# Optimization experiments

Measured on AMD Instinct MI355X. Metric: run time of the kernel, lower is better.

The kernel has to match this reference:

```python
import jax, jax.numpy as jnp
import numpy as np
from jax import lax
import math

C = 32            # num_channles
L_IN = 1024       # input signal length (forced by feature_size=520 constraint)
B = 1024          # batch


def _unfold(x, k, s):
    # x: (B, C, L) -> (B, C, n, k), torch Tensor.unfold(dim=2, size=k, step=s)
    n = (x.shape[-1] - k) // s + 1
    idx = np.arange(n)[:, None] * s + np.arange(k)[None, :]
    return x[..., idx]


def _always(x, w, b):
    # Conv1DAlwaysLayer: beta - sum_k (1 - window)*w, then relu, then leaky_relu(0.02)
    win = _unfold(x, 8, 2)                                  # (B,C,n,8)
    r = b[None, :, None] - jnp.einsum('bcnk,ck->bcn', 1.0 - win, w)
    return jax.nn.leaky_relu(jax.nn.relu(r), 0.02)


def _eventually(x, w, b):
    # Conv1DEventuallyLayer: relu(1 - (beta - sum_k window*w)), then leaky_relu(0.02)
    win = _unfold(x, 8, 2)
    r = 1.0 - (b[None, :, None] - jnp.einsum('bcnk,ck->bcn', win, w))
    return jax.nn.leaky_relu(jax.nn.relu(r), 0.02)


def _bn(x, g, b):
    # BatchNorm1d in training mode: batch statistics over (B, L), biased var
    m = x.mean(axis=(0, 2), keepdims=True)
    v = ((x - m) ** 2).mean(axis=(0, 2), keepdims=True)
    return (x - m) * jax.lax.rsqrt(v + 1e-5) * g[None, :, None] + b[None, :, None]


def _avgpool(x, k, s):
    return _unfold(x, k, s).mean(axis=-1)


def _maxpool(x, k, s):
    return _unfold(x, k, s).max(axis=-1)


def _laplace_filters(la_a, la_b):
    # LaplacePredicate filter bank: (C, 1, 16)
    A, ep, tal, f = 0.08, 0.03, 0.1, 50.0
    w = 2.0 * math.pi * f
    q = 1.0 - ep ** 2
    t = jnp.linspace(0.0, 1.0, 16, dtype=jnp.float32)       # kernel_size -> 16
    p = t[None, :] - (la_b / la_a)                           # (C,16)
    y = A * jnp.exp(-ep / math.sqrt(q) * (w * (p - tal))) * (-jnp.sin(w * (p - tal)))
    return y.reshape(C, 1, 16)


def setup_inputs() -> dict:
    key = jax.random.key(0)
    ks = jax.random.split(key, 32)
    rn = lambda k, shp: jax.random.normal(k, shp, dtype=jnp.float32)
    inp = {
        'x': rn(ks[0], (B, 1, L_IN)),
        # LaplacePredicate params
        'la_a': jnp.linspace(1.0, 10.0, C, dtype=jnp.float32).reshape(C, 1),
        'la_b': jnp.linspace(0.0, 10.0, C, dtype=jnp.float32).reshape(C, 1),
        'la_bias': rn(ks[1], (C,)),
        # BatchNorm after predicate
        'bn1_g': rn(ks[2], (C,)) * 0.1 + 1.0,
        'bn1_b': rn(ks[3], (C,)) * 0.1,
        # conv1d branch: Always -> Eventually -> MaxPool -> BN -> Eventually
        'a1_w': rn(ks[4], (C, 8)), 'a1_b': rn(ks[5], (C,)),
        'e1_w': rn(ks[6], (C, 8)), 'e1_b': rn(ks[7], (C,)),
        'bn2_g': rn(ks[8], (C,)) * 0.1 + 1.0, 'bn2_b': rn(ks[9], (C,)) * 0.1,
        'e2_w': rn(ks[10], (C, 8)), 'e2_b': rn(ks[11], (C,)),
        # conv1dFG branch: Eventually -> Always -> MaxPool -> BN -> Eventually
        'f1_w': rn(ks[12], (C, 8)), 'f1_b': rn(ks[13], (C,)),
        'fa_w': rn(ks[14], (C, 8)), 'fa_b': rn(ks[15], (C,)),
        'bn3_g': rn(ks[16], (C,)) * 0.1 + 1.0, 'bn3_b': rn(ks[17], (C,)) * 0.1,
        'f2_w': rn(ks[18], (C, 8)), 'f2_b': rn(ks[19], (C,)),
        # fc: 768 -> 1024 -> 512 -> 128 -> 10 (W stored (in,out))
        'w1': rn(ks[20], (768, 1024)) * (768 ** -0.5), 'b1': rn(ks[21], (1024,)) * 0.01,
        'w2': rn(ks[22], (1024, 512)) * (1024 ** -0.5), 'b2': rn(ks[23], (512,)) * 0.01,
        'w3': rn(ks[24], (512, 128)) * (512 ** -0.5), 'b3': rn(ks[25], (128,)) * 0.01,
        'w4': rn(ks[26], (128, 10)) * (128 ** -0.5), 'b4': rn(ks[27], (10,)) * 0.01,
    }
    return inp


def _forward(x, la_a, la_b, la_bias, bn1_g, bn1_b,
             a1_w, a1_b, e1_w, e1_b, bn2_g, bn2_b, e2_w, e2_b,
             f1_w, f1_b, fa_w, fa_b, bn3_g, bn3_b, f2_w, f2_b,
             w1, b1, w2, b2, w3, b3, w4, b4):
    # predicate_pos: LaplacePredicate -> BN -> AvgPool(3,2)
    filt = _laplace_filters(la_a, la_b)                      # (32,1,16)
    h = lax.conv_general_dilated(x, filt, window_strides=(1,),
                                 padding=[(16, 16)])         # (B,32,1041)
    h = h + la_bias[None, :, None]
    h = _bn(h, bn1_g, bn1_b)
    h = _avgpool(h, 3, 2)                                    # (B,32,520)
    # NOTE: fuseautoencoder/norm path in the source is dead code (result unused)
    # conv1d branch
    x1 = _always(h, a1_w, a1_b)                              # (B,32,257)
    x1 = _eventually(x1, e1_w, e1_b)                         # (B,32,125)
    x1 = _maxpool(x1, 4, 4)                                  # (B,32,31)
    x1 = _bn(x1, bn2_g, bn2_b)
    x1 = _eventually(x1, e2_w, e2_b)                         # (B,32,12)
    # conv1dFG branch
    x2 = _eventually(h, f1_w, f1_b)
    x2 = _always(x2, fa_w, fa_b)
    x2 = _maxpool(x2, 4, 4)
    x2 = _bn(x2, bn3_g, bn3_b)
    x2 = _eventually(x2, f2_w, f2_b)                         # (B,32,12)
    z = jnp.concatenate([x1, x2], axis=1).reshape(x.shape[0], -1)  # (B,768)
    z = jax.nn.relu(z @ w1 + b1)
    z = jax.nn.relu(z @ w2 + b2)    # Dropout -> identity (eval)
    z = jax.nn.relu(z @ w3 + b3)
    z = jax.nn.relu(z @ w4 + b4)
    return z                                                 # (B,10)


def reference(x, la_a, la_b, la_bias, bn1_g, bn1_b,
              a1_w, a1_b, e1_w, e1_b, bn2_g, bn2_b, e2_w, e2_b,
              f1_w, f1_b, fa_w, fa_b, bn3_g, bn3_b, f2_w, f2_b,
              w1, b1, w2, b2, w3, b3, w4, b4):
    return _forward(x, la_a, la_b, la_bias, bn1_g, bn1_b,
                    a1_w, a1_b, e1_w, e1_b, bn2_g, bn2_b, e2_w, e2_b,
                    f1_w, f1_b, fa_w, fa_b, bn3_g, bn3_b, f2_w, f2_b,
                    w1, b1, w2, b2, w3, b3, w4, b4)
```

## Files before the change

### kernel.cpp

```cpp
#include <hip/hip_runtime.h>
#include <math.h>


#define L_MP 31

using s8v = __attribute__((ext_vector_type(8))) short;
using f4v = __attribute__((ext_vector_type(4))) float;

__device__ __forceinline__ ushort f2bf(float f) {
    unsigned u = __float_as_uint(f);
    u += 0x7fffu + ((u >> 16) & 1u);
    return (ushort)(u >> 16);
}
__device__ __forceinline__ float bf2f(ushort u) {
    return __uint_as_float(((unsigned)u) << 16);
}

__global__ __launch_bounds__(256) void leaf_kernel(
    const float* __restrict__ x, double* __restrict__ xp,
    const float* __restrict__ w1, const float* __restrict__ w2,
    const float* __restrict__ w3,
    ushort* __restrict__ wt1, ushort* __restrict__ wt2, ushort* __restrict__ wt3)
{
    __shared__ __align__(16) float xr[1040];
    __shared__ float wred[4][17];
    __shared__ float tile[32][33];
    int bx = blockIdx.x, tid = threadIdx.x;

    if (bx < 1024) {
        int b = bx;
        for (int i = tid; i < 1024; i += 256) xr[i] = x[b * 1024 + i];
        if (tid < 16) xr[1024 + tid] = 0.f;
        __syncthreads();
        float acc[17];
#pragma unroll
        for (int d = 0; d < 17; ++d) acc[d] = 0.f;
        for (int p = tid; p < 1024; p += 256) {
            float v = xr[p];
            acc[16] += v;
#pragma unroll
            for (int d = 0; d < 16; ++d)
                acc[d] += v * xr[p + d];
        }
#pragma unroll
        for (int off = 32; off >= 1; off >>= 1)
#pragma unroll
            for (int d = 0; d < 17; ++d)
                acc[d] += __shfl_down(acc[d], off);
        int wave = tid >> 6, lane = tid & 63;
        if (lane == 0)
            for (int d = 0; d < 17; ++d) wred[wave][d] = acc[d];
        __syncthreads();
        if (tid < 17) {
            double tot = (double)wred[0][tid] + (double)wred[1][tid]
                       + (double)wred[2][tid] + (double)wred[3][tid];
            xp[tid * 1024 + b] = tot;
        }
    } else {
        int t2 = bx - 1024;
        const float* W; ushort* Wt; int K, N, ntx, tl;
        if (t2 < 768)       { W = w1; Wt = wt1; K = 768;  N = 1024; ntx = 32; tl = t2; }
        else if (t2 < 1280) { W = w2; Wt = wt2; K = 1024; N = 512;  ntx = 16; tl = t2 - 768; }
        else                { W = w3; Wt = wt3; K = 512;  N = 128;  ntx = 4;  tl = t2 - 1280; }
        int n0 = (tl % ntx) * 32, k0 = (tl / ntx) * 32;
        int tx = tid & 31, ty = tid >> 5;
#pragma unroll
        for (int i = 0; i < 4; ++i)
            tile[ty + 8 * i][tx] = W[(size_t)(k0 + ty + 8 * i) * N + n0 + tx];
        __syncthreads();
#pragma unroll
        for (int i = 0; i < 4; ++i)
            Wt[(size_t)(n0 + ty + 8 * i) * K + k0 + tx] = f2bf(tile[tx][ty + 8 * i]);
    }
}

__global__ __launch_bounds__(512) void prep_kernel(
    const double* __restrict__ xp,
    const float* __restrict__ la_a, const float* __restrict__ la_b,
    const float* __restrict__ bn1_g, const float* __restrict__ bn1_b,
    float* __restrict__ g18_out, float* __restrict__ a1d1_out)
{
    __shared__ double stats[17];
    __shared__ float fs[32][16];
    int tid = threadIdx.x, wv = tid >> 6, lane = tid & 63;

    for (int row = wv; row < 17; row += 8) {
        const double* r = xp + (size_t)row * 1024;
        double a = 0.0;
        for (int i = lane; i < 1024; i += 64) a += r[i];
#pragma unroll
        for (int off = 32; off >= 1; off >>= 1) a += __shfl_down(a, off);
        if (lane == 0) stats[row] = a;
    }

    {
        int c = tid >> 4, k = tid & 15;
        const double A = 0.08, ep = 0.03, tal = 0.1;
        const double w = 2.0 * 3.14159265358979323846 * 50.0;
        const double q = 1.0 - ep * ep;
        double t = (double)k / 15.0;
        double p = t - (double)la_b[c] / (double)la_a[c];
        double arg = w * (p - tal);
        double y = A * exp(-ep / sqrt(q) * arg) * (-sin(arg));
        fs[c][k] = (float)y;
    }
    __syncthreads();
    if (tid < 32) {
        int c = tid;
        for (int i = 0; i < 18; ++i) {
            float g = 0.f;
            for (int k = i - 2; k <= i; ++k)
                if (k >= 0 && k < 16) g += fs[c][k];
            g18_out[c * 18 + i] = g;
        }
        double Sf = 0.0;
        for (int k = 0; k < 16; ++k) Sf += (double)fs[c][k];
        double E2 = 0.0;
        for (int k = 0; k < 16; ++k)
            for (int k2 = 0; k2 < 16; ++k2)
                E2 += (double)fs[c][k] * (double)fs[c][k2]
                    * stats[k > k2 ? k - k2 : k2 - k];
        const double N = 1024.0 * 1041.0;
        double Sx = stats[16];
        double mc  = Sx * Sf / N;
        double var = E2 / N - mc * mc;
        double invstd = 1.0 / sqrt(var + 1e-5);
        float alpha = bn1_g[c] * (float)invstd;
        a1d1_out[c]      = alpha / 3.0f;
        a1d1_out[32 + c] = bn1_b[c] - (float)mc * alpha;
    }
}

__global__ __launch_bounds__(256) void branches_kernel(
    const float* __restrict__ x,
    const float* __restrict__ g18g, const float* __restrict__ a1d1,
    const float* __restrict__ a1w_g, const float* __restrict__ a1b_g,
    const float* __restrict__ e1w_g, const float* __restrict__ e1b_g,
    const float* __restrict__ f1w_g, const float* __restrict__ f1b_g,
    const float* __restrict__ faw_g, const float* __restrict__ fab_g,
    float* __restrict__ p1, float* __restrict__ p2)
{
    __shared__ float xs[1140];
    __shared__ float htail[16][6];

    int blk = blockIdx.x;
    int b = blk >> 1, hf = blk & 1;
    int t = threadIdx.x;
    int wv = t >> 6, lane = t & 63;

    {
        float4 v = ((const float4*)(x + (size_t)b * 1024))[t];
        int li = 16 + 4 * t;
        int ph = li + (li >> 4);
        xs[ph] = v.x; xs[ph + 1] = v.y; xs[ph + 2] = v.z; xs[ph + 3] = v.w;
        if (t < 16) xs[t] = 0.f;
        if (t < 32) { int i = 1040 + t; xs[i + (i >> 4)] = 0.f; }
    }
    __syncthreads();

    if (t < 96) {
        int cl = t / 6, e = t - 6 * (t / 6);
        int cg = hf * 16 + cl;
        float s = 0.f;
#pragma unroll
        for (int i = 0; i < 18; ++i) {
            int li = 1024 + 2 * e + i;
            s += g18g[cg * 18 + i] * xs[li + (li >> 4)];
        }
        htail[cl][e] = s * a1d1[cg] + a1d1[32 + cg];
    }
    __syncthreads();

    float xw[32];
    {
        int base = 17 * lane;
#pragma unroll
        for (int q = 0; q < 16; ++q) xw[q] = xs[base + q];
#pragma unroll
        for (int q = 0; q < 16; ++q) xw[16 + q] = xs[base + 17 + q];
    }

    for (int cc = 0; cc < 4; ++cc) {
        int cl = wv * 4 + cc;
        int cg = __builtin_amdgcn_readfirstlane(hf * 16 + cl);
        float alpha = a1d1[cg], delta = a1d1[32 + cg];

        float hv[8];
        {
            float g[18];
#pragma unroll
            for (int i = 0; i < 18; ++i) g[i] = g18g[cg * 18 + i];
#pragma unroll
            for (int jj = 0; jj < 8; ++jj) {
                float s = 0.f;
#pragma unroll
                for (int i = 0; i < 18; ++i) s += g[i] * xw[2 * jj + i];
                hv[jj] = s * alpha + delta;
            }
        }

        float x1v[4], x2v[4];
        {
            float hx[14];
#pragma unroll
            for (int q = 0; q < 8; ++q) hx[q] = hv[q];
#pragma unroll
            for (int q = 0; q < 6; ++q) {
                float u = __shfl_down(hv[q], 1);
                float tl = htail[cl][q];
                hx[8 + q] = (lane == 63) ? tl : u;
            }
            float wa[8], wf[8];
            float A1 = a1b_g[cg], F1 = 1.f - f1b_g[cg];
#pragma unroll
            for (int k = 0; k < 8; ++k) {
                wa[k] = a1w_g[cg * 8 + k];
                wf[k] = f1w_g[cg * 8 + k];
                A1 -= wa[k];
            }
#pragma unroll
            for (int nn = 0; nn < 4; ++nn) {
                float s1 = A1, s2 = F1;
#pragma unroll
                for (int k = 0; k < 8; ++k) {
                    float h = hx[2 * nn + k];
                    s1 += h * wa[k];
                    s2 += h * wf[k];
                }
                x1v[nn] = s1 > 0.f ? s1 : 0.f;
                x2v[nn] = s2 > 0.f ? s2 : 0.f;
            }
        }

        float y1v[2], y2v[2];
        {
            float xx1[10], xx2[10];
#pragma unroll
            for (int q = 0; q < 4; ++q) { xx1[q] = x1v[q]; xx2[q] = x2v[q]; }
#pragma unroll
            for (int q = 0; q < 4; ++q) {
                xx1[4 + q] = __shfl_down(x1v[q], 1);
                xx2[4 + q] = __shfl_down(x2v[q], 1);
            }
#pragma unroll
            for (int q = 0; q < 2; ++q) {
                xx1[8 + q] = __shfl_down(x1v[q], 2);
                xx2[8 + q] = __shfl_down(x2v[q], 2);
            }
            float we[8], wfa[8];
            float E1 = 1.f - e1b_g[cg], FA = fab_g[cg];
#pragma unroll
            for (int k = 0; k < 8; ++k) {
                we[k]  = e1w_g[cg * 8 + k];
                wfa[k] = faw_g[cg * 8 + k];
                FA -= wfa[k];
            }
#pragma unroll
            for (int mm = 0; mm < 2; ++mm) {
                float s1 = E1, s2 = FA;
#pragma unroll
                for (int k = 0; k < 8; ++k) {
                    s1 += xx1[2 * mm + k] * we[k];
                    s2 += xx2[2 * mm + k] * wfa[k];
                }
                y1v[mm] = s1 > 0.f ? s1 : 0.f;
                y2v[mm] = s2 > 0.f ? s2 : 0.f;
            }
        }

        {
            float m1 = fmaxf(y1v[0], y1v[1]);
            float m2 = fmaxf(y2v[0], y2v[1]);
            float n1 = __shfl_down(m1, 1);
            float n2 = __shfl_down(m2, 1);
            int tt = lane >> 1;
            if (!(lane & 1) && tt < L_MP) {
                int bc = b * 32 + hf * 16 + cl;
                p1[(size_t)bc * L_MP + tt] = fmaxf(m1, n1);
                p2[(size_t)bc * L_MP + tt] = fmaxf(m2, n2);
            }
        }
    }
}

__global__ __launch_bounds__(256) void pstats_kernel(
    const float* __restrict__ p1, const float* __restrict__ p2,
    double* __restrict__ bn_d)
{
    __shared__ double wr[4][2];
    int bx = blockIdx.x, arr = bx >> 5, c = bx & 31;
    const float* p = arr ? p2 : p1;
    int t = threadIdx.x, wv = t >> 6, lane = t & 63;
    double s = 0.0, q = 0.0;
    for (int bb = t; bb < 1024; bb += 256) {
        const float* r = p + ((size_t)bb * 32 + c) * L_MP;
#pragma unroll
        for (int j = 0; j < L_MP; ++j) {
            double v = (double)r[j];
            s += v; q += v * v;
        }
    }
#pragma unroll
    for (int off = 32; off >= 1; off >>= 1) {
        s += __shfl_down(s, off);
        q += __shfl_down(q, off);
    }
    if (lane == 0) { wr[wv][0] = s; wr[wv][1] = q; }
    __syncthreads();
    if (t == 0) {
        bn_d[arr * 64 + c]      = wr[0][0] + wr[1][0] + wr[2][0] + wr[3][0];
        bn_d[arr * 64 + 32 + c] = wr[0][1] + wr[1][1] + wr[2][1] + wr[3][1];
    }
}

__global__ __launch_bounds__(256) void final_ev_kernel(
    const float* __restrict__ p1, const float* __restrict__ p2,
    const float* __restrict__ e2w_g, const float* __restrict__ e2b_g,
    const float* __restrict__ f2w_g, const float* __restrict__ f2b_g,
    const double* __restrict__ bn_d,
    const float* __restrict__ bn2_g, const float* __restrict__ bn2_b,
    const float* __restrict__ bn3_g, const float* __restrict__ bn3_b,
    ushort* __restrict__ z0)
{
    __shared__ float pr[2][32][31];
    __shared__ float w2s[2][32][8];
    __shared__ float al[2][32], de[2][32], eb[2][32];
    int b = blockIdx.x, tid = threadIdx.x;
    for (int i = tid; i < 992; i += 256) {
        pr[0][0][i] = p1[b * 992 + i];
        pr[1][0][i] = p2[b * 992 + i];
    }
    {
        w2s[0][0][tid] = e2w_g[tid];
        w2s[1][0][tid] = f2w_g[tid];
    }
    if (tid < 64) {
        int br = tid >> 5, c = tid & 31;
        double sum = bn_d[br * 64 + c], sq = bn_d[br * 64 + 32 + c];
        const double N = 1024.0 * 31.0;
        double mean = sum / N;
        double var = sq / N - mean * mean;
        float g  = br ? bn3_g[c] : bn2_g[c];
        float be = br ? bn3_b[c] : bn2_b[c];
        float alpha = g * (float)(1.0 / sqrt(var + 1e-5));
        al[br][c] = alpha;
        de[br][c] = be - (float)mean * alpha;
        eb[br][c] = br ? f2b_g[c] : e2b_g[c];
    }
    __syncthreads();
    for (int u = tid; u < 768; u += 256) {
        int br = u / 384, rem = u - br * 384;
        int c = rem / 12, tt = rem - c * 12;
        float a = al[br][c], d = de[br][c];
        float s = 1.f - eb[br][c];
#pragma unroll
        for (int k = 0; k < 8; ++k)
            s += (pr[br][c][2 * tt + k] * a + d) * w2s[br][c][k];
        z0[(size_t)b * 768 + u] = f2bf(s > 0.f ? s : 0.f);
    }
}

template<int NT>
__global__ __launch_bounds__(256) void gemm_mfma_kernel(
    const ushort* __restrict__ A, const ushort* __restrict__ Bt,
    const float* __restrict__ bias, ushort* __restrict__ C,
    int N, int K)
{
    int w = blockIdx.x * 4 + (threadIdx.x >> 6);
    int lane = threadIdx.x & 63;
    int nstr = N / (16 * NT);
    int mt = w / nstr, ns = w - mt * nstr;
    int r = lane & 15, q = lane >> 4;
    const ushort* ap = A + (size_t)(mt * 16 + r) * K + q * 8;
    const ushort* bp[NT];
    f4v acc[NT];
#pragma unroll
    for (int u = 0; u < NT; ++u) {
        bp[u] = Bt + (size_t)(ns * 16 * NT + u * 16 + r) * K + q * 8;
        acc[u] = (f4v){0.f, 0.f, 0.f, 0.f};
    }
    int nk = K >> 5;
    s8v a0 = *(const s8v*)ap;
    s8v b0[NT];
#pragma unroll
    for (int u = 0; u < NT; ++u) b0[u] = *(const s8v*)bp[u];
#pragma unroll 4
    for (int i = 0; i < nk; ++i) {
        int j = (i + 1 < nk) ? i + 1 : i;
        s8v a1 = *(const s8v*)(ap + (size_t)j * 32);
        s8v b1[NT];
#pragma unroll
        for (int u = 0; u < NT; ++u) b1[u] = *(const s8v*)(bp[u] + (size_t)j * 32);
#pragma unroll
        for (int u = 0; u < NT; ++u)
            acc[u] = __builtin_amdgcn_mfma_f32_16x16x32_bf16(a0, b0[u], acc[u], 0, 0, 0);
        a0 = a1;
#pragma unroll
        for (int u = 0; u < NT; ++u) b0[u] = b1[u];
    }
    int row0 = mt * 16 + q * 4;
#pragma unroll
    for (int u = 0; u < NT; ++u) {
        int col = ns * 16 * NT + u * 16 + r;
        float bv = bias[col];
#pragma unroll
        for (int rr = 0; rr < 4; ++rr) {
            float v = acc[u][rr] + bv;
            v = v > 0.f ? v : 0.f;
            C[(size_t)(row0 + rr) * N + col] = f2bf(v);
        }
    }
}

__global__ __launch_bounds__(256) void gemm3_fc4_kernel(
    const ushort* __restrict__ A, const ushort* __restrict__ Bt,
    const float* __restrict__ bias, const float* __restrict__ w4,
    const float* __restrict__ b4, float* __restrict__ out)
{
    __shared__ ushort strip[16][132];
    const int K = 512, NCOL = 128;
    int blk = blockIdx.x;
    int wv = threadIdx.x >> 6, lane = threadIdx.x & 63;
    int r = lane & 15, q = lane >> 4;

    const ushort* ap  = A + (size_t)(blk * 16 + r) * K + q * 8;
    const ushort* bp0 = Bt + (size_t)(wv * 32 + r) * K + q * 8;
    const ushort* bp1 = Bt + (size_t)(wv * 32 + 16 + r) * K + q * 8;
    f4v acc0 = {0.f, 0.f, 0.f, 0.f}, acc1 = {0.f, 0.f, 0.f, 0.f};
    int nk = K >> 5;
    s8v a0 = *(const s8v*)ap;
    s8v c0 = *(const s8v*)bp0;
    s8v d0 = *(const s8v*)bp1;
#pragma unroll 4
    for (int i = 0; i < nk; ++i) {
        int j = (i + 1 < nk) ? i + 1 : i;
        s8v a1 = *(const s8v*)(ap + (size_t)j * 32);
        s8v c1 = *(const s8v*)(bp0 + (size_t)j * 32);
        s8v d1 = *(const s8v*)(bp1 + (size_t)j * 32);
        acc0 = __builtin_amdgcn_mfma_f32_16x16x32_bf16(a0, c0, acc0, 0, 0, 0);
        acc1 = __builtin_amdgcn_mfma_f32_16x16x32_bf16(a0, d0, acc1, 0, 0, 0);
        a0 = a1; c0 = c1; d0 = d1;
    }
    float bv0 = bias[wv * 32 + r], bv1 = bias[wv * 32 + 16 + r];
#pragma unroll
    for (int rr = 0; rr < 4; ++rr) {
        float v0 = acc0[rr] + bv0; v0 = v0 > 0.f ? v0 : 0.f;
        float v1 = acc1[rr] + bv1; v1 = v1 > 0.f ? v1 : 0.f;
        strip[q * 4 + rr][wv * 32 + r]      = f2bf(v0);
        strip[q * 4 + rr][wv * 32 + 16 + r] = f2bf(v1);
    }
    __syncthreads();

    int t = threadIdx.x;
    if (t < 160) {
        int m = t / 10, n = t - 10 * (t / 10);
        float a = b4[n];
#pragma unroll 8
        for (int k = 0; k < NCOL; ++k)
            a += bf2f(strip[m][k]) * w4[k * 10 + n];
        out[(size_t)(blk * 16 + m) * 10 + n] = a > 0.f ? a : 0.f;
    }
}

extern "C" void kernel_launch(void* const* d_in, const int* in_sizes, int n_in,
                              void* d_out, int out_size, void* d_ws, size_t ws_size,
                              hipStream_t stream)
{
    (void)in_sizes; (void)n_in; (void)out_size; (void)ws_size;
    const float* x      = (const float*)d_in[0];
    const float* la_a   = (const float*)d_in[1];
    const float* la_b   = (const float*)d_in[2];
    const float* bn1_g  = (const float*)d_in[4];
    const float* bn1_b  = (const float*)d_in[5];
    const float* a1_w   = (const float*)d_in[6];
    const float* a1_b   = (const float*)d_in[7];
    const float* e1_w   = (const float*)d_in[8];
    const float* e1_b   = (const float*)d_in[9];
    const float* bn2_g  = (const float*)d_in[10];
    const float* bn2_b  = (const float*)d_in[11];
    const float* e2_w   = (const float*)d_in[12];
    const float* e2_b   = (const float*)d_in[13];
    const float* f1_w   = (const float*)d_in[14];
    const float* f1_b   = (const float*)d_in[15];
    const float* fa_w   = (const float*)d_in[16];
    const float* fa_b   = (const float*)d_in[17];
    const float* bn3_g  = (const float*)d_in[18];
    const float* bn3_b  = (const float*)d_in[19];
    const float* f2_w   = (const float*)d_in[20];
    const float* f2_b   = (const float*)d_in[21];
    const float* w1     = (const float*)d_in[22];
    const float* b1     = (const float*)d_in[23];
    const float* w2     = (const float*)d_in[24];
    const float* b2     = (const float*)d_in[25];
    const float* w3     = (const float*)d_in[26];
    const float* b3     = (const float*)d_in[27];
    const float* w4     = (const float*)d_in[28];
    const float* b4     = (const float*)d_in[29];
    float* out = (float*)d_out;

    char* w = (char*)d_ws;
    double* bn_d    = (double*)(w + 256);
    float* g18      = (float*)(w + 1536);
    float* a1d1     = (float*)(w + 3840);
    float* p1       = (float*)(w + 8192);
    float* p2       = (float*)(w + 4071424);
    ushort* z0bf    = (ushort*)(w + 8134656);
    ushort* z1bf    = (ushort*)(w + 9707520);
    ushort* z2bf    = (ushort*)(w + 11804672);
    ushort* wt1     = (ushort*)(w + 13115392);
    ushort* wt2     = (ushort*)(w + 14688256);
    ushort* wt3     = (ushort*)(w + 15736832);
    double* xp      = (double*)(w + 15867904);

    leaf_kernel<<<2368, 256, 0, stream>>>(x, xp, w1, w2, w3, wt1, wt2, wt3);
    prep_kernel<<<1, 512, 0, stream>>>(xp, la_a, la_b, bn1_g, bn1_b, g18, a1d1);
    branches_kernel<<<2048, 256, 0, stream>>>(
        x, g18, a1d1, a1_w, a1_b, e1_w, e1_b, f1_w, f1_b, fa_w, fa_b, p1, p2);
    pstats_kernel<<<64, 256, 0, stream>>>(p1, p2, bn_d);
    final_ev_kernel<<<1024, 256, 0, stream>>>(
        p1, p2, e2_w, e2_b, f2_w, f2_b, bn_d, bn2_g, bn2_b, bn3_g, bn3_b, z0bf);
    gemm_mfma_kernel<2><<<512, 256, 0, stream>>>(z0bf, wt1, b1, z1bf, 1024, 768);
    gemm_mfma_kernel<1><<<512, 256, 0, stream>>>(z1bf, wt2, b2, z2bf, 512, 1024);
    gemm3_fc4_kernel<<<64, 256, 0, stream>>>(z2bf, wt3, b3, w4, b4, out);
}
```

Baseline: 219.3 us.

## Fuse final eventually layer and all FC layers into one LDS-resident kernel

Replaces the final_ev kernel, the two MFMA GEMM kernels and the gemm3+fc4 kernel with a single kernel. It launches 64 blocks of 1024 threads, and each block owns a 16-row batch tile. The intermediate activations z0, z1 and z2 stay in shared memory instead of round-tripping through global memory, which removes three launches. The cost is far fewer waves in flight: each block streams all the FC weights from L2 and builds its z0 tile serially over 16 rows with barriers, so the GPU is underoccupied.

```diff
diff --git a/kernel.cpp b/kernel.cpp
--- a/kernel.cpp
+++ b/kernel.cpp
@@ -313,29 +313,36 @@
     }
 }
 
-__global__ __launch_bounds__(256) void final_ev_kernel(
+__global__ __launch_bounds__(1024) void megafc_kernel(
     const float* __restrict__ p1, const float* __restrict__ p2,
     const float* __restrict__ e2w_g, const float* __restrict__ e2b_g,
     const float* __restrict__ f2w_g, const float* __restrict__ f2b_g,
     const double* __restrict__ bn_d,
     const float* __restrict__ bn2_g, const float* __restrict__ bn2_b,
     const float* __restrict__ bn3_g, const float* __restrict__ bn3_b,
-    ushort* __restrict__ z0)
+    const ushort* __restrict__ wt1, const float* __restrict__ b1,
+    const ushort* __restrict__ wt2, const float* __restrict__ b2,
+    const ushort* __restrict__ wt3, const float* __restrict__ b3,
+    const float* __restrict__ w4, const float* __restrict__ b4,
+    float* __restrict__ out)
 {
+    __shared__ __align__(16) ushort z0s[16][776];
+    __shared__ __align__(16) ushort z1s[16][1032];
+    __shared__ __align__(16) ushort z2s[16][520];
+    __shared__ __align__(16) ushort z3s[16][136];
     __shared__ float pr[2][32][31];
     __shared__ float w2s[2][32][8];
     __shared__ float al[2][32], de[2][32], eb[2][32];
-    int b = blockIdx.x, tid = threadIdx.x;
-    for (int i = tid; i < 992; i += 256) {
-        pr[0][0][i] = p1[b * 992 + i];
-        pr[1][0][i] = p2[b * 992 + i];
-    }
-    {
-        w2s[0][0][tid] = e2w_g[tid];
-        w2s[1][0][tid] = f2w_g[tid];
-    }
-    if (tid < 64) {
-        int br = tid >> 5, c = tid & 31;
+
+    int blk = blockIdx.x;
+    int t = threadIdx.x;
+    int wv = t >> 6, lane = t & 63;
+    int r = lane & 15, q = lane >> 4;
+
+    if (t < 256) { w2s[0][0][t] = e2w_g[t]; w2s[1][0][t] = f2w_g[t]; }
+    if (t >= 960) {
+        int tt = t - 960;
+        int br = tt >> 5, c = tt & 31;
         double sum = bn_d[br * 64 + c], sq = bn_d[br * 64 + 32 + c];
         const double N = 1024.0 * 31.0;
         double mean = sum / N;
@@ -348,116 +355,125 @@
         eb[br][c] = br ? f2b_g[c] : e2b_g[c];
     }
     __syncthreads();
-    for (int u = tid; u < 768; u += 256) {
-        int br = u / 384, rem = u - br * 384;
-        int c = rem / 12, tt = rem - c * 12;
-        float a = al[br][c], d = de[br][c];
-        float s = 1.f - eb[br][c];
-#pragma unroll
-        for (int k = 0; k < 8; ++k)
-            s += (pr[br][c][2 * tt + k] * a + d) * w2s[br][c][k];
-        z0[(size_t)b * 768 + u] = f2bf(s > 0.f ? s : 0.f);
-    }
-}
-
-template<int NT>
-__global__ __launch_bounds__(256) void gemm_mfma_kernel(
-    const ushort* __restrict__ A, const ushort* __restrict__ Bt,
-    const float* __restrict__ bias, ushort* __restrict__ C,
-    int N, int K)
-{
-    int w = blockIdx.x * 4 + (threadIdx.x >> 6);
-    int lane = threadIdx.x & 63;
-    int nstr = N / (16 * NT);
-    int mt = w / nstr, ns = w - mt * nstr;
-    int r = lane & 15, q = lane >> 4;
-    const ushort* ap = A + (size_t)(mt * 16 + r) * K + q * 8;
-    const ushort* bp[NT];
-    f4v acc[NT];
-#pragma unroll
-    for (int u = 0; u < NT; ++u) {
-        bp[u] = Bt + (size_t)(ns * 16 * NT + u * 16 + r) * K + q * 8;
-        acc[u] = (f4v){0.f, 0.f, 0.f, 0.f};
-    }
-    int nk = K >> 5;
-    s8v a0 = *(const s8v*)ap;
-    s8v b0[NT];
-#pragma unroll
-    for (int u = 0; u < NT; ++u) b0[u] = *(const s8v*)bp[u];
+
+    for (int bb = 0; bb < 16; ++bb) {
+        int gb = blk * 16 + bb;
+        if (t < 992) {
+            pr[0][0][t] = p1[(size_t)gb * 992 + t];
+            pr[1][0][t] = p2[(size_t)gb * 992 + t];
+        }
+        __syncthreads();
+        if (t < 768) {
+            int u = t;
+            int br = u / 384, rem = u - br * 384;
+            int c = rem / 12, tt = rem - c * 12;
+            float a = al[br][c], d = de[br][c];
+            float s = 1.f - eb[br][c];
+#pragma unroll
+            for (int k = 0; k < 8; ++k)
+                s += (pr[br][c][2 * tt + k] * a + d) * w2s[br][c][k];
+            z0s[bb][u] = f2bf(s > 0.f ? s : 0.f);
+        }
+        __syncthreads();
+    }
+
+#pragma unroll
+    for (int pp = 0; pp < 2; ++pp) {
+        int nt0 = wv * 4 + pp * 2;
+        const ushort* bpa = wt1 + (size_t)(nt0 * 16 + r) * 768 + q * 8;
+        const ushort* bpb = wt1 + (size_t)((nt0 + 1) * 16 + r) * 768 + q * 8;
+        const ushort* apl = &z0s[r][q * 8];
+        f4v ac0 = {0.f, 0.f, 0.f, 0.f}, ac1 = {0.f, 0.f, 0.f, 0.f};
+        s8v a0 = *(const s8v*)apl;
+        s8v c0 = *(const s8v*)bpa;
+        s8v d0 = *(const s8v*)bpb;
 #pragma unroll 4
-    for (int i = 0; i < nk; ++i) {
-        int j = (i + 1 < nk) ? i + 1 : i;
-        s8v a1 = *(const s8v*)(ap + (size_t)j * 32);
-        s8v b1[NT];
-#pragma unroll
-        for (int u = 0; u < NT; ++u) b1[u] = *(const s8v*)(bp[u] + (size_t)j * 32);
-#pragma unroll
-        for (int u = 0; u < NT; ++u)
-            acc[u] = __builtin_amdgcn_mfma_f32_16x16x32_bf16(a0, b0[u], acc[u], 0, 0, 0);
-        a0 = a1;
-#pragma unroll
-        for (int u = 0; u < NT; ++u) b0[u] = b1[u];
-    }
-    int row0 = mt * 16 + q * 4;
-#pragma unroll
-    for (int u = 0; u < NT; ++u) {
-        int col = ns * 16 * NT + u * 16 + r;
-        float bv = bias[col];
+        for (int i = 0; i < 24; ++i) {
+            int j = (i + 1 < 24) ? i + 1 : i;
+            s8v a1 = *(const s8v*)(apl + j * 32);
+            s8v c1 = *(const s8v*)(bpa + (size_t)j * 32);
+            s8v d1 = *(const s8v*)(bpb + (size_t)j * 32);
+            ac0 = __builtin_amdgcn_mfma_f32_16x16x32_bf16(a0, c0, ac0, 0, 0, 0);
+            ac1 = __builtin_amdgcn_mfma_f32_16x16x32_bf16(a0, d0, ac1, 0, 0, 0);
+            a0 = a1; c0 = c1; d0 = d1;
+        }
+        float bv0 = b1[nt0 * 16 + r], bv1 = b1[(nt0 + 1) * 16 + r];
 #pragma unroll
         for (int rr = 0; rr < 4; ++rr) {
-            float v = acc[u][rr] + bv;
-            v = v > 0.f ? v : 0.f;
-            C[(size_t)(row0 + rr) * N + col] = f2bf(v);
-        }
-    }
-}
-
-__global__ __launch_bounds__(256) void gemm3_fc4_kernel(
-    const ushort* __restrict__ A, const ushort* __restrict__ Bt,
-    const float* __restrict__ bias, const float* __restrict__ w4,
-    const float* __restrict__ b4, float* __restrict__ out)
-{
-    __shared__ ushort strip[16][132];
-    const int K = 512, NCOL = 128;
-    int blk = blockIdx.x;
-    int wv = threadIdx.x >> 6, lane = threadIdx.x & 63;
-    int r = lane & 15, q = lane >> 4;
-
-    const ushort* ap  = A + (size_t)(blk * 16 + r) * K + q * 8;
-    const ushort* bp0 = Bt + (size_t)(wv * 32 + r) * K + q * 8;
-    const ushort* bp1 = Bt + (size_t)(wv * 32 + 16 + r) * K + q * 8;
-    f4v acc0 = {0.f, 0.f, 0.f, 0.f}, acc1 = {0.f, 0.f, 0.f, 0.f};
-    int nk = K >> 5;
-    s8v a0 = *(const s8v*)ap;
-    s8v c0 = *(const s8v*)bp0;
-    s8v d0 = *(const s8v*)bp1;
+            float v0 = ac0[rr] + bv0; v0 = v0 > 0.f ? v0 : 0.f;
+            float v1 = ac1[rr] + bv1; v1 = v1 > 0.f ? v1 : 0.f;
+            z1s[q * 4 + rr][nt0 * 16 + r]       = f2bf(v0);
+            z1s[q * 4 + rr][(nt0 + 1) * 16 + r] = f2bf(v1);
+        }
+    }
+    __syncthreads();
+
+    {
+        int nt0 = wv * 2;
+        const ushort* bpa = wt2 + (size_t)(nt0 * 16 + r) * 1024 + q * 8;
+        const ushort* bpb = wt2 + (size_t)((nt0 + 1) * 16 + r) * 1024 + q * 8;
+        const ushort* apl = &z1s[r][q * 8];
+        f4v ac0 = {0.f, 0.f, 0.f, 0.f}, ac1 = {0.f, 0.f, 0.f, 0.f};
+        s8v a0 = *(const s8v*)apl;
+        s8v c0 = *(const s8v*)bpa;
+        s8v d0 = *(const s8v*)bpb;
 #pragma unroll 4
-    for (int i = 0; i < nk; ++i) {
-        int j = (i + 1 < nk) ? i + 1 : i;
-        s8v a1 = *(const s8v*)(ap + (size_t)j * 32);
-        s8v c1 = *(const s8v*)(bp0 + (size_t)j * 32);
-        s8v d1 = *(const s8v*)(bp1 + (size_t)j * 32);
-        acc0 = __builtin_amdgcn_mfma_f32_16x16x32_bf16(a0, c0, acc0, 0, 0, 0);
-        acc1 = __builtin_amdgcn_mfma_f32_16x16x32_bf16(a0, d0, acc1, 0, 0, 0);
-        a0 = a1; c0 = c1; d0 = d1;
-    }
-    float bv0 = bias[wv * 32 + r], bv1 = bias[wv * 32 + 16 + r];
-#pragma unroll
-    for (int rr = 0; rr < 4; ++rr) {
-        float v0 = acc0[rr] + bv0; v0 = v0 > 0.f ? v0 : 0.f;
-        float v1 = acc1[rr] + bv1; v1 = v1 > 0.f ? v1 : 0.f;
-        strip[q * 4 + rr][wv * 32 + r]      = f2bf(v0);
-        strip[q * 4 + rr][wv * 32 + 16 + r] = f2bf(v1);
-    }
-    __syncthreads();
-
-    int t = threadIdx.x;
+        for (int i = 0; i < 32; ++i) {
+            int j = (i + 1 < 32) ? i + 1 : i;
+            s8v a1 = *(const s8v*)(apl + j * 32);
+            s8v c1 = *(const s8v*)(bpa + (size_t)j * 32);
+            s8v d1 = *(const s8v*)(bpb + (size_t)j * 32);
+            ac0 = __builtin_amdgcn_mfma_f32_16x16x32_bf16(a0, c0, ac0, 0, 0, 0);
+            ac1 = __builtin_amdgcn_mfma_f32_16x16x32_bf16(a0, d0, ac1, 0, 0, 0);
+            a0 = a1; c0 = c1; d0 = d1;
+        }
+        float bv0 = b2[nt0 * 16 + r], bv1 = b2[(nt0 + 1) * 16 + r];
+#pragma unroll
+        for (int rr = 0; rr < 4; ++rr) {
+            float v0 = ac0[rr] + bv0; v0 = v0 > 0.f ? v0 : 0.f;
+            float v1 = ac1[rr] + bv1; v1 = v1 > 0.f ? v1 : 0.f;
+            z2s[q * 4 + rr][nt0 * 16 + r]       = f2bf(v0);
+            z2s[q * 4 + rr][(nt0 + 1) * 16 + r] = f2bf(v1);
+        }
+    }
+    __syncthreads();
+
+    if (wv < 4) {
+        int nt0 = wv * 2;
+        const ushort* bpa = wt3 + (size_t)(nt0 * 16 + r) * 512 + q * 8;
+        const ushort* bpb = wt3 + (size_t)((nt0 + 1) * 16 + r) * 512 + q * 8;
+        const ushort* apl = &z2s[r][q * 8];
+        f4v ac0 = {0.f, 0.f, 0.f, 0.f}, ac1 = {0.f, 0.f, 0.f, 0.f};
+        s8v a0 = *(const s8v*)apl;
+        s8v c0 = *(const s8v*)bpa;
+        s8v d0 = *(const s8v*)bpb;
+#pragma unroll 4
+        for (int i = 0; i < 16; ++i) {
+            int j = (i + 1 < 16) ? i + 1 : i;
+            s8v a1 = *(const s8v*)(apl + j * 32);
+            s8v c1 = *(const s8v*)(bpa + (size_t)j * 32);
+            s8v d1 = *(const s8v*)(bpb + (size_t)j * 32);
+            ac0 = __builtin_amdgcn_mfma_f32_16x16x32_bf16(a0, c0, ac0, 0, 0, 0);
+            ac1 = __builtin_amdgcn_mfma_f32_16x16x32_bf16(a0, d0, ac1, 0, 0, 0);
+            a0 = a1; c0 = c1; d0 = d1;
+        }
+        float bv0 = b3[nt0 * 16 + r], bv1 = b3[(nt0 + 1) * 16 + r];
+#pragma unroll
+        for (int rr = 0; rr < 4; ++rr) {
+            float v0 = ac0[rr] + bv0; v0 = v0 > 0.f ? v0 : 0.f;
+            float v1 = ac1[rr] + bv1; v1 = v1 > 0.f ? v1 : 0.f;
+            z3s[q * 4 + rr][nt0 * 16 + r]       = f2bf(v0);
+            z3s[q * 4 + rr][(nt0 + 1) * 16 + r] = f2bf(v1);
+        }
+    }
+    __syncthreads();
+
     if (t < 160) {
         int m = t / 10, n = t - 10 * (t / 10);
         float a = b4[n];
 #pragma unroll 8
-        for (int k = 0; k < NCOL; ++k)
-            a += bf2f(strip[m][k]) * w4[k * 10 + n];
+        for (int k = 0; k < 128; ++k)
+            a += bf2f(z3s[m][k]) * w4[k * 10 + n];
         out[(size_t)(blk * 16 + m) * 10 + n] = a > 0.f ? a : 0.f;
     }
 }
@@ -504,9 +520,6 @@
     float* a1d1     = (float*)(w + 3840);
     float* p1       = (float*)(w + 8192);
     float* p2       = (float*)(w + 4071424);
-    ushort* z0bf    = (ushort*)(w + 8134656);
-    ushort* z1bf    = (ushort*)(w + 9707520);
-    ushort* z2bf    = (ushort*)(w + 11804672);
     ushort* wt1     = (ushort*)(w + 13115392);
     ushort* wt2     = (ushort*)(w + 14688256);
     ushort* wt3     = (ushort*)(w + 15736832);
@@ -517,9 +530,7 @@
     branches_kernel<<<2048, 256, 0, stream>>>(
         x, g18, a1d1, a1_w, a1_b, e1_w, e1_b, f1_w, f1_b, fa_w, fa_b, p1, p2);
     pstats_kernel<<<64, 256, 0, stream>>>(p1, p2, bn_d);
-    final_ev_kernel<<<1024, 256, 0, stream>>>(
-        p1, p2, e2_w, e2_b, f2_w, f2_b, bn_d, bn2_g, bn2_b, bn3_g, bn3_b, z0bf);
-    gemm_mfma_kernel<2><<<512, 256, 0, stream>>>(z0bf, wt1, b1, z1bf, 1024, 768);
-    gemm_mfma_kernel<1><<<512, 256, 0, stream>>>(z1bf, wt2, b2, z2bf, 512, 1024);
-    gemm3_fc4_kernel<<<64, 256, 0, stream>>>(z2bf, wt3, b3, w4, b4, out);
-}
+    megafc_kernel<<<64, 1024, 0, stream>>>(
+        p1, p2, e2_w, e2_b, f2_w, f2_b, bn_d, bn2_g, bn2_b, bn3_g, bn3_b,
+        wt1, b1, wt2, b2, wt3, b3, w4, b4, out);
+}
```

After: 263.6 us. 1.2x slower.
